# Kernel optimization log

Measured on AMD Instinct MI355X. Metric: run time of the kernel, lower is better.

The kernel has to match this reference:

```python
import jax, jax.numpy as jnp
import numpy as np
from jax import lax

START_TAG = 29
STOP_TAG = 30
PAD_TAG = 31
NEG_INF = -10000.0


def setup_inputs() -> dict:
    key = jax.random.key(0)
    k_feat, k_trans, k_len = jax.random.split(key, 3)
    S, B, T = 1024, 1024, 32
    feats = jax.random.normal(k_feat, (S, B, T), dtype=jnp.float32)
    # left-aligned padding mask with random lengths in [S//2, S]
    lengths = jax.random.randint(k_len, (B,), S // 2, S + 1)
    mask = (jnp.arange(S)[:, None] < lengths[None, :]).astype(jnp.float32)  # [S,B]
    transitions = jax.random.normal(k_trans, (T, T), dtype=jnp.float32)
    # replicate the constraint initialization from __init__
    transitions = transitions.at[START_TAG, :].set(NEG_INF)
    transitions = transitions.at[:, STOP_TAG].set(NEG_INF)
    transitions = transitions.at[:, PAD_TAG].set(NEG_INF)
    transitions = transitions.at[PAD_TAG, :].set(NEG_INF)
    transitions = transitions.at[PAD_TAG, STOP_TAG].set(0.0)
    transitions = transitions.at[PAD_TAG, PAD_TAG].set(0.0)
    # zero emissions at padded steps, as _get_lstm_features does (feats * mask)
    feats = feats * mask[:, :, None]
    return {"feats": feats, "mask": mask, "transitions": transitions}


def reference(feats, mask, transitions):
    """CRF forward algorithm (log partition) + Viterbi max-score scan.

    feats: [S, B, T] emission scores, mask: [S, B] float, transitions: [T, T]
    (transitions[i, j] = score of transitioning from tag j to tag i).
    Returns (logZ [B], best_score [B], pointers [S, B, T] int32).
    """
    S, B, T = feats.shape

    alpha0 = jnp.full((B, T), NEG_INF, dtype=feats.dtype).at[:, START_TAG].set(0.0)

    def fwd_step(alpha, xs):
        feat, m = xs  # feat [B,T], m [B]
        # alpha_t[b, i, j] = alpha[b, j] + transitions[i, j] + feat[b, i]
        alpha_t = alpha[:, None, :] + transitions[None, :, :] + feat[:, :, None]
        new = jax.nn.logsumexp(alpha_t, axis=-1)  # [B,T]
        m = m[:, None]
        return new * m + alpha * (1.0 - m), None

    alpha, _ = lax.scan(fwd_step, alpha0, (feats, mask))
    logZ = jax.nn.logsumexp(alpha + transitions[STOP_TAG][None, :], axis=-1)  # [B]

    def vit_step(scores, xs):
        feat, m = xs
        scores_t = scores[:, None, :] + transitions[None, :, :]  # [B,T,T]
        best = jnp.max(scores_t, axis=-1)                        # [B,T]
        ptr = jnp.argmax(scores_t, axis=-1).astype(jnp.int32)    # [B,T]
        scores_t = best + feat
        m = m[:, None]
        return scores_t * m + scores * (1.0 - m), ptr

    scores0 = jnp.full((B, T), NEG_INF, dtype=feats.dtype).at[:, START_TAG].set(0.0)
    scores, pointers = lax.scan(vit_step, scores0, (feats, mask))
    scores = scores + transitions[STOP_TAG][None, :]
    best_score = jnp.max(scores, axis=-1)  # [B]
    return logZ, best_score, pointers
```

## Files before the change

kernel.cpp:

```cpp
#include <hip/hip_runtime.h>


#define SS 1024
#define BB 1024
#define TT 32
#define POFF (2 * BB)

static __device__ __forceinline__ float fastrcp(float x) {
#if __has_builtin(__builtin_amdgcn_rcpf)
  return __builtin_amdgcn_rcpf(x);
#else
  return 1.0f / x;
#endif
}

#define DPP_QX1   0xB1
#define DPP_QX2   0x4E
#define DPP_QX3   0x1B
#define DPP_RMIR  0x140
#define DPP_RHMIR 0x141

template <int CTRL>
static __device__ __forceinline__ float dppx(float x) {
  return __int_as_float(
      __builtin_amdgcn_update_dpp(0, __float_as_int(x), CTRL, 0xF, 0xF, false));
}

static __device__ __forceinline__ float bperm(int byteaddr, float x) {
  return __int_as_float(
      __builtin_amdgcn_ds_bpermute(byteaddr, __float_as_int(x)));
}

static __device__ __forceinline__ float swap32(float x, bool hiHalf) {
#if __has_builtin(__builtin_amdgcn_permlane32_swap)
  auto r = __builtin_amdgcn_permlane32_swap(__float_as_uint(x),
                                            __float_as_uint(x), false, false);
  return __uint_as_float(hiHalf ? r[0] : r[1]);
#else
  float a = x, b = x;
  asm("s_nop 1\n\ts_nop 1\n\tv_permlane32_swap_b32 %0, %1"
      : "+v"(a), "+v"(b));
  return hiHalf ? a : b;
#endif
}

static __device__ __forceinline__ void gather16(float x, float r[16]) {
  r[0]  = x;
  r[1]  = dppx<DPP_QX1>(x);
  r[2]  = dppx<DPP_QX2>(x);
  r[3]  = dppx<DPP_QX3>(x);
  r[7]  = dppx<DPP_RHMIR>(x);
  r[6]  = dppx<DPP_QX1>(r[7]);
  r[5]  = dppx<DPP_QX2>(r[7]);
  r[4]  = dppx<DPP_QX3>(r[7]);
  r[15] = dppx<DPP_RMIR>(x);
  r[14] = dppx<DPP_QX1>(r[15]);
  r[13] = dppx<DPP_QX2>(r[15]);
  r[12] = dppx<DPP_QX3>(r[15]);
  r[8]  = dppx<DPP_RHMIR>(r[15]);
  r[9]  = dppx<DPP_QX1>(r[8]);
  r[10] = dppx<DPP_QX2>(r[8]);
  r[11] = dppx<DPP_QX3>(r[8]);
}

__global__ __launch_bounds__(64, 1) void crf5_kernel(
    const float* __restrict__ feats,
    const float* __restrict__ mask,
    const float* __restrict__ trans,
    float* __restrict__ out) {

  const int l  = threadIdx.x;
  const int t0 = l & 15;
  const int i  = t0 | ((l >> 1) & 16);
  const int h  = (l >> 4) & 1;
  const int b0 = blockIdx.x * 2;
  const int b  = b0 + h;
  const bool hiHalf = (l & 32) != 0;

  const float* fbase = feats + (size_t)b * TT + i;
  const float* mbase = mask + b;
  const float t_stop = trans[30 * TT + i];

  float fA[4], mA[4], fB[4], mB[4];
#pragma unroll
  for (int u = 0; u < 4; ++u) {
    fA[u] = fbase[(size_t)u * (BB * TT)];
    mA[u] = mbase[(size_t)u * BB];
    fB[u] = fbase[(size_t)(u + 4) * (BB * TT)];
    mB[u] = mbase[(size_t)(u + 4) * BB];
  }

  if (blockIdx.y == 0) {
    float eOwn[16], eOth[16];
#pragma unroll
    for (int m = 0; m < 16; ++m) {
      int x = t0 ^ m;
      int jown = hiHalf ? (16 | x) : x;
      int joth = hiHalf ? x : (16 | x);
      eOwn[m] = __expf(trans[i * TT + jown]);
      eOth[m] = __expf(trans[i * TT + joth]);
    }

    float p   = (i == 29) ? 1.0f : 0.0f;
    float C   = 0.0f;
    float q0f = 0.0f;

    auto fstep = [&](float fv, float mv) {
      bool act = (mv != 0.0f);
      float ef  = __expf(fv);
      float q0c = fmaxf(q0f, 1e-20f);
      float scale = fastrcp(q0c) * ef;
      float r16[16];
      gather16(p, r16);
      float y = swap32(p, hiHalf);
      float o16[16];
      gather16(y, o16);
      float a0 = eOwn[0] * r16[0], a1 = eOwn[1] * r16[1];
      float a2 = eOwn[2] * r16[2], a3 = eOwn[3] * r16[3];
#pragma unroll
      for (int m = 4; m < 16; m += 4) {
        a0 = fmaf(eOwn[m + 0], r16[m + 0], a0);
        a1 = fmaf(eOwn[m + 1], r16[m + 1], a1);
        a2 = fmaf(eOwn[m + 2], r16[m + 2], a2);
        a3 = fmaf(eOwn[m + 3], r16[m + 3], a3);
      }
#pragma unroll
      for (int m = 0; m < 16; m += 4) {
        a0 = fmaf(eOth[m + 0], o16[m + 0], a0);
        a1 = fmaf(eOth[m + 1], o16[m + 1], a1);
        a2 = fmaf(eOth[m + 2], o16[m + 2], a2);
        a3 = fmaf(eOth[m + 3], o16[m + 3], a3);
      }
      float D  = (a0 + a1) + (a2 + a3);
      float pn = D * scale;
      p = act ? pn : p;
      C += act ? __logf(q0c) : 0.0f;
      q0f = bperm((l & 16) << 2, p);
    };

#pragma unroll 1
    for (int s = 0; s < SS; s += 8) {
      if (__ballot(mA[0] != 0.0f) == 0ull) goto fwd_done;
#pragma unroll
      for (int u = 0; u < 4; ++u) fstep(fA[u], mA[u]);
#pragma unroll
      for (int u = 0; u < 4; ++u) {
        int su = s + 8 + u; su = (su < SS) ? su : 0;
        fA[u] = fbase[(size_t)su * (BB * TT)];
        mA[u] = mbase[(size_t)su * BB];
      }
      if (__ballot(mB[0] != 0.0f) == 0ull) goto fwd_done;
#pragma unroll
      for (int u = 0; u < 4; ++u) fstep(fB[u], mB[u]);
#pragma unroll
      for (int u = 0; u < 4; ++u) {
        int su = s + 12 + u; su = (su < SS) ? su : 0;
        fB[u] = fbase[(size_t)su * (BB * TT)];
        mB[u] = mbase[(size_t)su * BB];
      }
    }
fwd_done:
    {
      float alpha = C + __logf(p);
      float v = alpha + t_stop;
      float M2 = v;
      M2 = fmaxf(M2, __shfl_xor(M2, 1, 64));
      M2 = fmaxf(M2, __shfl_xor(M2, 2, 64));
      M2 = fmaxf(M2, __shfl_xor(M2, 4, 64));
      M2 = fmaxf(M2, __shfl_xor(M2, 8, 64));
      M2 = fmaxf(M2, __shfl_xor(M2, 32, 64));
      float e = __expf(v - M2);
      e += __shfl_xor(e, 1, 64);
      e += __shfl_xor(e, 2, 64);
      e += __shfl_xor(e, 4, 64);
      e += __shfl_xor(e, 8, 64);
      e += __shfl_xor(e, 32, 64);
      if (i == 0) out[b] = M2 + __logf(e);
    }
    return;
  }

  {
    float    tOwn[16], tOth[16];
    unsigned bOwn[16], bOth[16];
#pragma unroll
    for (int m = 0; m < 16; ++m) {
      int x = t0 ^ m;
      int jown = hiHalf ? (16 | x) : x;
      int joth = hiHalf ? x : (16 | x);
      tOwn[m] = trans[i * TT + jown];
      tOth[m] = trans[i * TT + joth];
      bOwn[m] = 1u << jown;
      bOth[m] = 1u << joth;
    }

    float sc = (i == 29) ? 0.0f : -10000.0f;
    int s_exit = SS;
    float* outp = out + POFF + (size_t)b * TT + i;

    auto vstep = [&](float& best, int& ptr) {
      float r16[16];
      gather16(sc, r16);
      float y = swap32(sc, hiHalf);
      float o16[16];
      gather16(y, o16);
      float vv[32];
#pragma unroll
      for (int m = 0; m < 16; ++m) vv[m] = r16[m] + tOwn[m];
#pragma unroll
      for (int m = 0; m < 16; ++m) vv[16 + m] = o16[m] + tOth[m];
      float g[11];
#pragma unroll
      for (int k = 0; k < 10; ++k)
        g[k] = fmaxf(fmaxf(vv[3 * k], vv[3 * k + 1]), vv[3 * k + 2]);
      g[10] = fmaxf(vv[30], vv[31]);
      float h0 = fmaxf(fmaxf(g[0], g[1]), g[2]);
      float h1 = fmaxf(fmaxf(g[3], g[4]), g[5]);
      float h2 = fmaxf(fmaxf(g[6], g[7]), g[8]);
      float h3 = fmaxf(g[9], g[10]);
      float mx = fmaxf(fmaxf(fmaxf(h0, h1), h2), h3);
      unsigned msk = 0u;
#pragma unroll
      for (int m = 0; m < 16; ++m) msk |= (vv[m] == mx) ? bOwn[m] : 0u;
#pragma unroll
      for (int m = 0; m < 16; ++m) msk |= (vv[16 + m] == mx) ? bOth[m] : 0u;
      best = mx;
      ptr  = __ffs(msk) - 1;
    };

#pragma unroll 1
    for (int s = 0; s < SS; s += 8) {
      if (__ballot(mA[0] != 0.0f) == 0ull) { s_exit = s; goto vtail; }
#pragma unroll
      for (int u2 = 0; u2 < 4; ++u2) {
        float best; int ptr;
        vstep(best, ptr);
        outp[(size_t)(s + u2) * (BB * TT)] = (float)ptr;
        sc = (mA[u2] != 0.0f) ? (best + fA[u2]) : sc;
      }
#pragma unroll
      for (int u2 = 0; u2 < 4; ++u2) {
        int su = s + 8 + u2; su = (su < SS) ? su : 0;
        fA[u2] = fbase[(size_t)su * (BB * TT)];
        mA[u2] = mbase[(size_t)su * BB];
      }
      if (__ballot(mB[0] != 0.0f) == 0ull) { s_exit = s + 4; goto vtail; }
#pragma unroll
      for (int u2 = 0; u2 < 4; ++u2) {
        float best; int ptr;
        vstep(best, ptr);
        outp[(size_t)(s + 4 + u2) * (BB * TT)] = (float)ptr;
        sc = (mB[u2] != 0.0f) ? (best + fB[u2]) : sc;
      }
#pragma unroll
      for (int u2 = 0; u2 < 4; ++u2) {
        int su = s + 12 + u2; su = (su < SS) ? su : 0;
        fB[u2] = fbase[(size_t)su * (BB * TT)];
        mB[u2] = mbase[(size_t)su * BB];
      }
    }
vtail:
    {
      float tb; int tp;
      vstep(tb, tp);
      float tj = (float)tp;
      for (int s2 = s_exit; s2 < SS; ++s2)
        outp[(size_t)s2 * (BB * TT)] = tj;

      float w = sc + t_stop;
      w = fmaxf(w, __shfl_xor(w, 1, 64));
      w = fmaxf(w, __shfl_xor(w, 2, 64));
      w = fmaxf(w, __shfl_xor(w, 4, 64));
      w = fmaxf(w, __shfl_xor(w, 8, 64));
      w = fmaxf(w, __shfl_xor(w, 32, 64));
      if (i == 0) out[BB + b] = w;
    }
  }
}

extern "C" void kernel_launch(void* const* d_in, const int* in_sizes, int n_in,
                              void* d_out, int out_size, void* d_ws, size_t ws_size,
                              hipStream_t stream) {
  const float* feats = (const float*)d_in[0];
  const float* msk   = (const float*)d_in[1];
  const float* trans = (const float*)d_in[2];
  float* out = (float*)d_out;
  (void)in_sizes; (void)n_in; (void)out_size; (void)d_ws; (void)ws_size;
  crf5_kernel<<<dim3(BB / 2, 2), dim3(64), 0, stream>>>(feats, msk, trans, out);
}
```

Before: 631.1 us.

## Split each tag's 32-way reduction across two half-waves, one batch per wave

Each wave now handles one batch element instead of two. Every tag row is split across two 32-lane halves that each reduce over 16 source tags, and the halves are combined with a permlane32 swap. The forward pass replaces the reciprocal/log normalisation with exponent-only power-of-two scaling taken from a readfirstlane value, and accumulates an integer exponent count. The change doubles the number of waves and halves the serial per-step reduction depth, at the cost of extra cross-lane swaps and twice as many workgroups.

```diff
diff --git a/kernel.cpp b/kernel.cpp
--- a/kernel.cpp
+++ b/kernel.cpp
@@ -5,14 +5,6 @@
 #define BB 1024
 #define TT 32
 #define POFF (2 * BB)
-
-static __device__ __forceinline__ float fastrcp(float x) {
-#if __has_builtin(__builtin_amdgcn_rcpf)
-  return __builtin_amdgcn_rcpf(x);
-#else
-  return 1.0f / x;
-#endif
-}
 
 #define DPP_QX1   0xB1
 #define DPP_QX2   0x4E
@@ -24,11 +16,6 @@
 static __device__ __forceinline__ float dppx(float x) {
   return __int_as_float(
       __builtin_amdgcn_update_dpp(0, __float_as_int(x), CTRL, 0xF, 0xF, false));
-}
-
-static __device__ __forceinline__ float bperm(int byteaddr, float x) {
-  return __int_as_float(
-      __builtin_amdgcn_ds_bpermute(byteaddr, __float_as_int(x)));
 }
 
 static __device__ __forceinline__ float swap32(float x, bool hiHalf) {
@@ -41,6 +28,19 @@
   asm("s_nop 1\n\ts_nop 1\n\tv_permlane32_swap_b32 %0, %1"
       : "+v"(a), "+v"(b));
   return hiHalf ? a : b;
+#endif
+}
+
+static __device__ __forceinline__ float swap16(float x, bool hi16) {
+#if __has_builtin(__builtin_amdgcn_permlane16_swap)
+  auto r = __builtin_amdgcn_permlane16_swap(__float_as_uint(x),
+                                            __float_as_uint(x), false, false);
+  return __uint_as_float(hi16 ? r[0] : r[1]);
+#else
+  float a = x, b = x;
+  asm("s_nop 1\n\ts_nop 1\n\tv_permlane16_swap_b32 %0, %1"
+      : "+v"(a), "+v"(b));
+  return hi16 ? a : b;
 #endif
 }
 
@@ -63,19 +63,20 @@
   r[11] = dppx<DPP_QX3>(r[8]);
 }
 
-__global__ __launch_bounds__(64, 1) void crf5_kernel(
+__global__ __launch_bounds__(64, 2) void crf6_kernel(
     const float* __restrict__ feats,
     const float* __restrict__ mask,
     const float* __restrict__ trans,
     float* __restrict__ out) {
 
-  const int l  = threadIdx.x;
-  const int t0 = l & 15;
-  const int i  = t0 | ((l >> 1) & 16);
-  const int h  = (l >> 4) & 1;
-  const int b0 = blockIdx.x * 2;
-  const int b  = b0 + h;
-  const bool hiHalf = (l & 32) != 0;
+  const int l   = threadIdx.x;
+  const int t0  = l & 15;
+  const int row = l >> 4;
+  const int i   = ((row & 1) << 4) | t0;
+  const int srcbase = (row == 1 || row == 2) ? 16 : 0;
+  const bool hi16   = (row & 1) != 0;
+  const bool hiHalf = (row & 2) != 0;
+  const int b = blockIdx.x;
 
   const float* fbase = feats + (size_t)b * TT + i;
   const float* mbase = mask + b;
@@ -91,56 +92,46 @@
   }
 
   if (blockIdx.y == 0) {
-    float eOwn[16], eOth[16];
-#pragma unroll
-    for (int m = 0; m < 16; ++m) {
-      int x = t0 ^ m;
-      int jown = hiHalf ? (16 | x) : x;
-      int joth = hiHalf ? x : (16 | x);
-      eOwn[m] = __expf(trans[i * TT + jown]);
-      eOth[m] = __expf(trans[i * TT + joth]);
-    }
+    float eT[16];
+#pragma unroll
+    for (int m = 0; m < 16; ++m)
+      eT[m] = __expf(trans[i * TT + (srcbase | (t0 ^ m))]);
 
     float p   = (i == 29) ? 1.0f : 0.0f;
-    float C   = 0.0f;
-    float q0f = 0.0f;
+    int   CE  = 0;
+    float q0f = 1.0f;
 
     auto fstep = [&](float fv, float mv) {
       bool act = (mv != 0.0f);
-      float ef  = __expf(fv);
-      float q0c = fmaxf(q0f, 1e-20f);
-      float scale = fastrcp(q0c) * ef;
+      float ef = __expf(fv);
+      int Eb = (int)((__float_as_uint(q0f) >> 23) & 0xFFu);
+      float scl = __uint_as_float((unsigned)(254 - Eb) << 23);
+      float efs = ef * scl;
+      float z = swap16(p, hi16);
+      float basev = hiHalf ? z : p;
       float r16[16];
-      gather16(p, r16);
-      float y = swap32(p, hiHalf);
-      float o16[16];
-      gather16(y, o16);
-      float a0 = eOwn[0] * r16[0], a1 = eOwn[1] * r16[1];
-      float a2 = eOwn[2] * r16[2], a3 = eOwn[3] * r16[3];
+      gather16(basev, r16);
+      float a0 = eT[0] * r16[0], a1 = eT[1] * r16[1];
+      float a2 = eT[2] * r16[2], a3 = eT[3] * r16[3];
 #pragma unroll
       for (int m = 4; m < 16; m += 4) {
-        a0 = fmaf(eOwn[m + 0], r16[m + 0], a0);
-        a1 = fmaf(eOwn[m + 1], r16[m + 1], a1);
-        a2 = fmaf(eOwn[m + 2], r16[m + 2], a2);
-        a3 = fmaf(eOwn[m + 3], r16[m + 3], a3);
-      }
-#pragma unroll
-      for (int m = 0; m < 16; m += 4) {
-        a0 = fmaf(eOth[m + 0], o16[m + 0], a0);
-        a1 = fmaf(eOth[m + 1], o16[m + 1], a1);
-        a2 = fmaf(eOth[m + 2], o16[m + 2], a2);
-        a3 = fmaf(eOth[m + 3], o16[m + 3], a3);
-      }
-      float D  = (a0 + a1) + (a2 + a3);
-      float pn = D * scale;
-      p = act ? pn : p;
-      C += act ? __logf(q0c) : 0.0f;
-      q0f = bperm((l & 16) << 2, p);
+        a0 = fmaf(eT[m + 0], r16[m + 0], a0);
+        a1 = fmaf(eT[m + 1], r16[m + 1], a1);
+        a2 = fmaf(eT[m + 2], r16[m + 2], a2);
+        a3 = fmaf(eT[m + 3], r16[m + 3], a3);
+      }
+      float Dp = (a0 + a1) + (a2 + a3);
+      float Df = Dp + swap32(Dp, hiHalf);
+      float pn = Df * efs;
+      p   = act ? pn : p;
+      CE += act ? (Eb - 127) : 0;
+      q0f = __uint_as_float(
+          (unsigned)__builtin_amdgcn_readfirstlane((int)__float_as_uint(p)));
     };
 
 #pragma unroll 1
     for (int s = 0; s < SS; s += 8) {
-      if (__ballot(mA[0] != 0.0f) == 0ull) goto fwd_done;
+      if (mA[0] == 0.0f) goto fwd_done;
 #pragma unroll
       for (int u = 0; u < 4; ++u) fstep(fA[u], mA[u]);
 #pragma unroll
@@ -149,7 +140,7 @@
         fA[u] = fbase[(size_t)su * (BB * TT)];
         mA[u] = mbase[(size_t)su * BB];
       }
-      if (__ballot(mB[0] != 0.0f) == 0ull) goto fwd_done;
+      if (mB[0] == 0.0f) goto fwd_done;
 #pragma unroll
       for (int u = 0; u < 4; ++u) fstep(fB[u], mB[u]);
 #pragma unroll
@@ -161,37 +152,33 @@
     }
 fwd_done:
     {
-      float alpha = C + __logf(p);
+      float alpha = (float)CE * 0.693147180559945f + __logf(p);
       float v = alpha + t_stop;
       float M2 = v;
       M2 = fmaxf(M2, __shfl_xor(M2, 1, 64));
       M2 = fmaxf(M2, __shfl_xor(M2, 2, 64));
       M2 = fmaxf(M2, __shfl_xor(M2, 4, 64));
       M2 = fmaxf(M2, __shfl_xor(M2, 8, 64));
-      M2 = fmaxf(M2, __shfl_xor(M2, 32, 64));
+      M2 = fmaxf(M2, __shfl_xor(M2, 16, 64));
       float e = __expf(v - M2);
       e += __shfl_xor(e, 1, 64);
       e += __shfl_xor(e, 2, 64);
       e += __shfl_xor(e, 4, 64);
       e += __shfl_xor(e, 8, 64);
-      e += __shfl_xor(e, 32, 64);
-      if (i == 0) out[b] = M2 + __logf(e);
+      e += __shfl_xor(e, 16, 64);
+      if (l == 0) out[b] = M2 + __logf(e);
     }
     return;
   }
 
   {
-    float    tOwn[16], tOth[16];
-    unsigned bOwn[16], bOth[16];
+    float tT[16];
+    int   tg[16];
 #pragma unroll
     for (int m = 0; m < 16; ++m) {
-      int x = t0 ^ m;
-      int jown = hiHalf ? (16 | x) : x;
-      int joth = hiHalf ? x : (16 | x);
-      tOwn[m] = trans[i * TT + jown];
-      tOth[m] = trans[i * TT + joth];
-      bOwn[m] = 1u << jown;
-      bOth[m] = 1u << joth;
+      int j = srcbase | (t0 ^ m);
+      tT[m] = trans[i * TT + j];
+      tg[m] = j;
     }
 
     float sc = (i == 29) ? 0.0f : -10000.0f;
@@ -199,43 +186,42 @@
     float* outp = out + POFF + (size_t)b * TT + i;
 
     auto vstep = [&](float& best, int& ptr) {
+      float z = swap16(sc, hi16);
+      float basev = hiHalf ? z : sc;
       float r16[16];
-      gather16(sc, r16);
-      float y = swap32(sc, hiHalf);
-      float o16[16];
-      gather16(y, o16);
-      float vv[32];
-#pragma unroll
-      for (int m = 0; m < 16; ++m) vv[m] = r16[m] + tOwn[m];
-#pragma unroll
-      for (int m = 0; m < 16; ++m) vv[16 + m] = o16[m] + tOth[m];
-      float g[11];
-#pragma unroll
-      for (int k = 0; k < 10; ++k)
-        g[k] = fmaxf(fmaxf(vv[3 * k], vv[3 * k + 1]), vv[3 * k + 2]);
-      g[10] = fmaxf(vv[30], vv[31]);
-      float h0 = fmaxf(fmaxf(g[0], g[1]), g[2]);
-      float h1 = fmaxf(fmaxf(g[3], g[4]), g[5]);
-      float h2 = fmaxf(fmaxf(g[6], g[7]), g[8]);
-      float h3 = fmaxf(g[9], g[10]);
-      float mx = fmaxf(fmaxf(fmaxf(h0, h1), h2), h3);
-      unsigned msk = 0u;
-#pragma unroll
-      for (int m = 0; m < 16; ++m) msk |= (vv[m] == mx) ? bOwn[m] : 0u;
-#pragma unroll
-      for (int m = 0; m < 16; ++m) msk |= (vv[16 + m] == mx) ? bOth[m] : 0u;
+      gather16(basev, r16);
+      float vv[16];
+#pragma unroll
+      for (int m = 0; m < 16; ++m) vv[m] = r16[m] + tT[m];
+      float g0 = fmaxf(fmaxf(vv[0], vv[1]), vv[2]);
+      float g1 = fmaxf(fmaxf(vv[3], vv[4]), vv[5]);
+      float g2 = fmaxf(fmaxf(vv[6], vv[7]), vv[8]);
+      float g3 = fmaxf(fmaxf(vv[9], vv[10]), vv[11]);
+      float g4 = fmaxf(fmaxf(vv[12], vv[13]), vv[14]);
+      float h0 = fmaxf(fmaxf(g0, g1), g2);
+      float h1 = fmaxf(fmaxf(g3, g4), vv[15]);
+      float mxp = fmaxf(h0, h1);
+      float mx = fmaxf(mxp, swap32(mxp, hiHalf));
+      int idx = 63;
+#pragma unroll
+      for (int m = 0; m < 16; ++m) {
+        int cand = (vv[m] == mx) ? tg[m] : 63;
+        idx = (cand < idx) ? cand : idx;
+      }
+      int oidx = __float_as_int(swap32(__int_as_float(idx), hiHalf));
+      idx = (oidx < idx) ? oidx : idx;
       best = mx;
-      ptr  = __ffs(msk) - 1;
+      ptr  = idx;
     };
 
 #pragma unroll 1
     for (int s = 0; s < SS; s += 8) {
-      if (__ballot(mA[0] != 0.0f) == 0ull) { s_exit = s; goto vtail; }
+      if (mA[0] == 0.0f) { s_exit = s; goto vtail; }
 #pragma unroll
       for (int u2 = 0; u2 < 4; ++u2) {
         float best; int ptr;
         vstep(best, ptr);
-        outp[(size_t)(s + u2) * (BB * TT)] = (float)ptr;
+        if (l < 32) outp[(size_t)(s + u2) * (BB * TT)] = (float)ptr;
         sc = (mA[u2] != 0.0f) ? (best + fA[u2]) : sc;
       }
 #pragma unroll
@@ -244,12 +230,12 @@
         fA[u2] = fbase[(size_t)su * (BB * TT)];
         mA[u2] = mbase[(size_t)su * BB];
       }
-      if (__ballot(mB[0] != 0.0f) == 0ull) { s_exit = s + 4; goto vtail; }
+      if (mB[0] == 0.0f) { s_exit = s + 4; goto vtail; }
 #pragma unroll
       for (int u2 = 0; u2 < 4; ++u2) {
         float best; int ptr;
         vstep(best, ptr);
-        outp[(size_t)(s + 4 + u2) * (BB * TT)] = (float)ptr;
+        if (l < 32) outp[(size_t)(s + 4 + u2) * (BB * TT)] = (float)ptr;
         sc = (mB[u2] != 0.0f) ? (best + fB[u2]) : sc;
       }
 #pragma unroll
@@ -265,15 +251,15 @@
       vstep(tb, tp);
       float tj = (float)tp;
       for (int s2 = s_exit; s2 < SS; ++s2)
-        outp[(size_t)s2 * (BB * TT)] = tj;
+        if (l < 32) outp[(size_t)s2 * (BB * TT)] = tj;
 
       float w = sc + t_stop;
       w = fmaxf(w, __shfl_xor(w, 1, 64));
       w = fmaxf(w, __shfl_xor(w, 2, 64));
       w = fmaxf(w, __shfl_xor(w, 4, 64));
       w = fmaxf(w, __shfl_xor(w, 8, 64));
-      w = fmaxf(w, __shfl_xor(w, 32, 64));
-      if (i == 0) out[BB + b] = w;
+      w = fmaxf(w, __shfl_xor(w, 16, 64));
+      if (l == 0) out[BB + b] = w;
     }
   }
 }
@@ -286,5 +272,5 @@
   const float* trans = (const float*)d_in[2];
   float* out = (float*)d_out;
   (void)in_sizes; (void)n_in; (void)out_size; (void)d_ws; (void)ws_size;
-  crf5_kernel<<<dim3(BB / 2, 2), dim3(64), 0, stream>>>(feats, msk, trans, out);
-}
+  crf6_kernel<<<dim3(BB, 2), dim3(64), 0, stream>>>(feats, msk, trans, out);
+}
```

Result: faster. 562.0 us (-10.9%).
